# Optimization experiments

Hardware: AMD Instinct MI355X
Metric: run time of the kernel (lower is better)

Reference implementation:

```python
import jax, jax.numpy as jnp
from jax import lax
import numpy as np

B, FRAMES, H, W = 8, 128, 64, 64
N_MFCC = 60
VID_FEAT = 196
D = VID_FEAT + N_MFCC   # COMBINE_SIZE = 256
ED = 2 * D              # mamba d_inner = 512
NST = 16                # d_state
DTR = 16                # dt_rank = ceil(D/16)
NL = 4                  # layers per direction
NC = 2                  # num_classes


def setup_inputs() -> dict:
    key = jax.random.key(0)
    ks = iter(jax.random.split(key, 64))
    def rn(shape, s=0.02):
        return jax.random.normal(next(ks), shape, jnp.float32) * s
    inp = {
        'video_input': jax.random.normal(next(ks), (B, FRAMES, 3, H, W), jnp.float32),
        'audio_input': jax.random.normal(next(ks), (B, FRAMES * N_MFCC), jnp.float32),
        'cnn_conv1_w': rn((32, 3, 3, 3), 0.1), 'cnn_conv1_b': jnp.zeros((32,), jnp.float32),
        'cnn_conv2_w': rn((64, 32, 3, 3), 0.05), 'cnn_conv2_b': jnp.zeros((64,), jnp.float32),
        'cnn_fc_w': rn((VID_FEAT, 64), 0.1), 'cnn_fc_b': jnp.zeros((VID_FEAT,), jnp.float32),
    }
    for pref in ('fwd', 'bwd'):
        inp[pref + '_norm_w'] = jnp.ones((NL, D), jnp.float32)
        inp[pref + '_in_proj_w'] = rn((NL, 2 * ED, D))
        inp[pref + '_conv_w'] = rn((NL, ED, 4), 0.1)
        inp[pref + '_conv_b'] = jnp.zeros((NL, ED), jnp.float32)
        inp[pref + '_x_proj_w'] = rn((NL, DTR + 2 * NST, ED))
        inp[pref + '_dt_w'] = rn((NL, ED, DTR), 0.1)
        inp[pref + '_dt_b'] = jnp.zeros((NL, ED), jnp.float32)
        inp[pref + '_A_log'] = jnp.tile(jnp.log(jnp.arange(1, NST + 1, dtype=jnp.float32)), (NL, ED, 1))
        inp[pref + '_D'] = jnp.ones((NL, ED), jnp.float32)
        inp[pref + '_out_proj_w'] = rn((NL, D, ED))
    inp['fc_w'] = rn((D, 2 * D)); inp['fc_b'] = jnp.zeros((D,), jnp.float32)
    inp['fc2_w'] = rn((NC, D)); inp['fc2_b'] = jnp.zeros((NC,), jnp.float32)
    return inp


def _rmsnorm(x, w, eps=1e-5):
    return x * lax.rsqrt(jnp.mean(x * x, -1, keepdims=True) + eps) * w


def _conv2d(x, w, b):
    y = lax.conv_general_dilated(x, w, (1, 1), 'SAME', dimension_numbers=('NCHW', 'OIHW', 'NCHW'))
    return y + b[None, :, None, None]


def _maxpool2(x):
    return lax.reduce_window(x, -jnp.inf, lax.max, (1, 1, 2, 2), (1, 1, 2, 2), 'VALID')


def _video_cnn(x, w1, b1, w2, b2, fw, fb):
    x = _maxpool2(jax.nn.relu(_conv2d(x, w1, b1)))
    x = _maxpool2(jax.nn.relu(_conv2d(x, w2, b2)))
    x = jnp.mean(x, (2, 3))            # global avg pool -> [B*F, 64]
    return x @ fw.T + fb               # [B*F, VID_FEAT]


def _mamba_layer(x, norm_w, in_w, conv_w, conv_b, xp_w, dt_w, dt_b, A_log, Dp, out_w):
    Bsz, L, _ = x.shape
    xn = _rmsnorm(x, norm_w)
    xz = jnp.einsum('bld,ed->ble', xn, in_w)        # [B,L,2*ED]
    xc, z = jnp.split(xz, 2, axis=-1)
    # causal depthwise conv1d, kernel 4
    xpad = jnp.pad(xc, ((0, 0), (3, 0), (0, 0)))
    xc = sum(xpad[:, k:k + L, :] * conv_w[:, k] for k in range(4)) + conv_b
    xc = jax.nn.silu(xc)
    dbc = jnp.einsum('ble,re->blr', xc, xp_w)       # [B,L,DTR+2*NST]
    dt, Bm, Cm = dbc[..., :DTR], dbc[..., DTR:DTR + NST], dbc[..., DTR + NST:]
    delta = jax.nn.softplus(jnp.einsum('blr,er->ble', dt, dt_w) + dt_b)  # [B,L,ED]
    A = -jnp.exp(A_log)                             # [ED,NST]
    dA = jnp.exp(delta[..., None] * A)              # [B,L,ED,NST]
    dBx = delta[..., None] * Bm[:, :, None, :] * xc[..., None]
    def step(h, inp):
        dA_t, dBx_t, c_t = inp
        h = dA_t * h + dBx_t
        return h, jnp.einsum('ben,bn->be', h, c_t)
    h0 = jnp.zeros((Bsz, ED, NST), x.dtype)
    _, ys = lax.scan(step, h0, (dA.transpose(1, 0, 2, 3), dBx.transpose(1, 0, 2, 3), Cm.transpose(1, 0, 2)))
    y = ys.transpose(1, 0, 2) + Dp * xc
    y = y * jax.nn.silu(z)
    return x + jnp.einsum('ble,de->bld', y, out_w)


def _mamba(x, norm_w, in_w, conv_w, conv_b, xp_w, dt_w, dt_b, A_log, Dp, out_w):
    for l in range(NL):
        x = _mamba_layer(x, norm_w[l], in_w[l], conv_w[l], conv_b[l], xp_w[l],
                         dt_w[l], dt_b[l], A_log[l], Dp[l], out_w[l])
    return x


def reference(video_input, audio_input, cnn_conv1_w, cnn_conv1_b, cnn_conv2_w, cnn_conv2_b,
              cnn_fc_w, cnn_fc_b,
              fwd_norm_w, fwd_in_proj_w, fwd_conv_w, fwd_conv_b, fwd_x_proj_w, fwd_dt_w,
              fwd_dt_b, fwd_A_log, fwd_D, fwd_out_proj_w,
              bwd_norm_w, bwd_in_proj_w, bwd_conv_w, bwd_conv_b, bwd_x_proj_w, bwd_dt_w,
              bwd_dt_b, bwd_A_log, bwd_D, bwd_out_proj_w,
              fc_w, fc_b, fc2_w, fc2_b):
    bsz, frames = video_input.shape[0], video_input.shape[1]
    xv = video_input.reshape(bsz * frames, 3, H, W)
    xv = _video_cnn(xv, cnn_conv1_w, cnn_conv1_b, cnn_conv2_w, cnn_conv2_b, cnn_fc_w, cnn_fc_b)
    xv = xv.reshape(bsz, frames, VID_FEAT)
    xa = audio_input.reshape(bsz, -1, N_MFCC)       # [B, frames, N_MFCC]
    xc = jnp.concatenate([xv, xa], axis=-1)         # [B, frames, D]
    xf = _mamba(xc, fwd_norm_w, fwd_in_proj_w, fwd_conv_w, fwd_conv_b, fwd_x_proj_w,
                fwd_dt_w, fwd_dt_b, fwd_A_log, fwd_D, fwd_out_proj_w)
    xb = _mamba(xc[:, ::-1], bwd_norm_w, bwd_in_proj_w, bwd_conv_w, bwd_conv_b, bwd_x_proj_w,
                bwd_dt_w, bwd_dt_b, bwd_A_log, bwd_D, bwd_out_proj_w)[:, ::-1]
    x_last = jnp.concatenate([xf, xb], axis=-1)[:, -1, :]   # [B, 2*D]; dropout = identity (eval)
    x = x_last @ fc_w.T + fc_b
    return x @ fc2_w.T + fc2_b
```

## Files before the change

kernel.cpp:

```cpp
#include <hip/hip_runtime.h>
#include <hip/hip_bf16.h>
#include <cstdint>
#include <cstddef>

#define BATCH 8
#define FRAMES 128
#define TOK (BATCH*FRAMES)
#define NM 60
#define VF 196
#define DD 256
#define EDIM 512
#define NSTATE 16
#define DTRANK 16
#define NLAYER 4

typedef __attribute__((ext_vector_type(8))) short short8v;
typedef __attribute__((ext_vector_type(4))) float f32x4;

__device__ __forceinline__ unsigned short f2bf(float f) {
  unsigned x = __float_as_uint(f);
  unsigned r = (x + 0x7FFFu + ((x >> 16) & 1u)) >> 16;
  return (unsigned short)r;
}

__global__ void pack_w2(const float* __restrict__ w2, unsigned short* __restrict__ Wb,
                        const float* __restrict__ w1, unsigned short* __restrict__ Wb1) {
  int id = blockIdx.x * 256 + threadIdx.x;
  if (id < 9 * 4 * 64) {
    int lane = id & 63;
    int mt = (id >> 6) & 3;
    int sh = id >> 8;
    int dy = sh / 3, dx = sh % 3;
    int oc = mt * 16 + (lane & 15);
    int ic0 = (lane >> 4) * 8;
    unsigned u[4];
#pragma unroll
    for (int p = 0; p < 4; ++p) {
      unsigned short lo = f2bf(w2[((oc * 32 + ic0 + 2 * p) * 3 + dy) * 3 + dx]);
      unsigned short hi = f2bf(w2[((oc * 32 + ic0 + 2 * p + 1) * 3 + dy) * 3 + dx]);
      u[p] = (unsigned)lo | ((unsigned)hi << 16);
    }
    uint4 v = {u[0], u[1], u[2], u[3]};
    *(uint4*)(Wb + (size_t)id * 8) = v;
  } else if (id < 9 * 4 * 64 + 128) {
    int id2 = id - 9 * 4 * 64;
    int mt = id2 >> 6, lane = id2 & 63;
    int oc = mt * 16 + (lane & 15);
    int ko = lane >> 4;
    unsigned u[4];
#pragma unroll
    for (int p = 0; p < 4; ++p) {
      int k0 = ko * 8 + 2 * p, k1 = k0 + 1;
      unsigned short lo = (k0 < 27) ? f2bf(w1[oc * 27 + k0]) : 0;
      unsigned short hi = (k1 < 27) ? f2bf(w1[oc * 27 + k1]) : 0;
      u[p] = (unsigned)lo | ((unsigned)hi << 16);
    }
    uint4 v = {u[0], u[1], u[2], u[3]};
    *(uint4*)(Wb1 + (size_t)id2 * 8) = v;
  }
}

__global__ void pack_mamba(const float* __restrict__ ipF, const float* __restrict__ ipR,
                           const float* __restrict__ opF, const float* __restrict__ opR,
                           const float* __restrict__ xpF, const float* __restrict__ xpR,
                           unsigned short* __restrict__ Wip, unsigned short* __restrict__ Wop,
                           unsigned short* __restrict__ Wxp) {
  int id = blockIdx.x * 256 + threadIdx.x;
  if (id < 262144) {
    int dl = id >> 15, r = id & 32767;
    int ntile = r >> 9, kt = (r >> 6) & 7, lane = r & 63;
    int dir = dl >> 2, layer = dl & 3;
    const float* src = (dir ? ipR : ipF) + (size_t)layer * 1024 * 256
                       + (size_t)(ntile * 16 + (lane & 15)) * 256 + kt * 32 + (lane >> 4) * 8;
    unsigned u[4];
#pragma unroll
    for (int p = 0; p < 4; ++p)
      u[p] = (unsigned)f2bf(src[2 * p]) | ((unsigned)f2bf(src[2 * p + 1]) << 16);
    uint4 v = {u[0], u[1], u[2], u[3]};
    *(uint4*)(Wip + (size_t)id * 8) = v;
  } else if (id < 262144 + 131072) {
    int id2 = id - 262144;
    int dl = id2 >> 14, rr = id2 & 16383;
    int ntile = rr >> 10, kt = (rr >> 6) & 15, lane = rr & 63;
    int dir = dl >> 2, layer = dl & 3;
    const float* src = (dir ? opR : opF) + (size_t)layer * 256 * 512
                       + (size_t)(ntile * 16 + (lane & 15)) * 512 + kt * 32 + (lane >> 4) * 8;
    unsigned u[4];
#pragma unroll
    for (int p = 0; p < 4; ++p)
      u[p] = (unsigned)f2bf(src[2 * p]) | ((unsigned)f2bf(src[2 * p + 1]) << 16);
    uint4 v = {u[0], u[1], u[2], u[3]};
    *(uint4*)(Wop + (size_t)id2 * 8) = v;
  } else if (id < 262144 + 131072 + 24576) {
    int id3 = id - 262144 - 131072;
    int dl = id3 / 3072, rr = id3 % 3072;
    int ntile = rr >> 10, kt = (rr >> 6) & 15, lane = rr & 63;
    int dir = dl >> 2, layer = dl & 3;
    const float* src = (dir ? xpR : xpF) + (size_t)layer * 48 * 512
                       + (size_t)(ntile * 16 + (lane & 15)) * 512 + kt * 32 + (lane >> 4) * 8;
    unsigned u[4];
#pragma unroll
    for (int p = 0; p < 4; ++p)
      u[p] = (unsigned)f2bf(src[2 * p]) | ((unsigned)f2bf(src[2 * p + 1]) << 16);
    uint4 v = {u[0], u[1], u[2], u[3]};
    *(uint4*)(Wxp + (size_t)id3 * 8) = v;
  }
}

#define C1RS 68
#define C1ICS (66*68)
__global__ __launch_bounds__(256) void conv1_mfma(
    const float* __restrict__ video, const unsigned short* __restrict__ Wb1,
    const float* __restrict__ b1, unsigned short* __restrict__ X1)
{
  __shared__ unsigned short ldsu[3 * C1ICS + 96];
  const int img = blockIdx.x, t = threadIdx.x;
  const float* vin = video + (size_t)img * 12288;
  const int lane = t & 63, wv = t >> 6;
  const int col = lane & 15, ko = lane >> 4;

  for (int i = t; i < (3 * C1ICS + 96) / 2; i += 256) ((unsigned*)ldsu)[i] = 0;
  __syncthreads();
#pragma unroll
  for (int i = 0; i < 12; ++i) {
    int c = i * 256 + t;
    int ic = c >> 10, rem = c & 1023, gy = rem >> 4, c4 = rem & 15;
    float4 v = *(const float4*)(vin + ic * 4096 + gy * 64 + c4 * 4);
    unsigned lo = (unsigned)f2bf(v.x) | ((unsigned)f2bf(v.y) << 16);
    unsigned hi = (unsigned)f2bf(v.z) | ((unsigned)f2bf(v.w) << 16);
    int di = ic * C1ICS + (gy + 1) * C1RS + 4 + c4 * 4;
    *(uint2*)(ldsu + di) = (uint2){lo, hi};
  }

  short8v A0 = *(const short8v*)(Wb1 + (size_t)(0 * 64 + lane) * 8);
  short8v A1 = *(const short8v*)(Wb1 + (size_t)(1 * 64 + lane) * 8);
  float bia[2][4];
#pragma unroll
  for (int mt = 0; mt < 2; ++mt)
#pragma unroll
    for (int r = 0; r < 4; ++r) bia[mt][r] = b1[mt * 16 + ko * 4 + r];

  int offs[8];
#pragma unroll
  for (int j = 0; j < 8; ++j) {
    int k = ko * 8 + j;
    int o = 0;
    if (k < 27) {
      int ic = k / 9, tap = k - ic * 9;
      int dy = tap / 3, dx = tap - dy * 3;
      o = ic * C1ICS + dy * C1RS + dx + 3;
    }
    offs[j] = o;
  }
  __syncthreads();

  f32x4 z4 = {0.f, 0.f, 0.f, 0.f};
#pragma unroll 1
  for (int rp = 0; rp < 8; ++rp) {
    const int y0 = wv * 16 + rp * 2;
#pragma unroll
    for (int xg = 0; xg < 4; ++xg) {
      const int bse = y0 * C1RS + xg * 16 + col;
      short8v vb0, vb1;
#pragma unroll
      for (int j = 0; j < 8; ++j) {
        vb0[j] = (short)ldsu[bse + offs[j]];
        vb1[j] = (short)ldsu[bse + C1RS + offs[j]];
      }
      f32x4 c00 = __builtin_amdgcn_mfma_f32_16x16x32_bf16(A0, vb0, z4, 0, 0, 0);
      f32x4 c10 = __builtin_amdgcn_mfma_f32_16x16x32_bf16(A1, vb0, z4, 0, 0, 0);
      f32x4 c01 = __builtin_amdgcn_mfma_f32_16x16x32_bf16(A0, vb1, z4, 0, 0, 0);
      f32x4 c11 = __builtin_amdgcn_mfma_f32_16x16x32_bf16(A1, vb1, z4, 0, 0, 0);
      const int py = wv * 8 + rp;
      const int pxp = xg * 8 + (col >> 1);
#pragma unroll
      for (int mt = 0; mt < 2; ++mt) {
        f32x4 ca = mt ? c10 : c00;
        f32x4 cb = mt ? c11 : c01;
        unsigned pk[2];
#pragma unroll
        for (int r = 0; r < 4; ++r) {
          float va = fmaxf(ca[r] + bia[mt][r], 0.f);
          float vb = fmaxf(cb[r] + bia[mt][r], 0.f);
          float v = fmaxf(va, vb);
          v = fmaxf(v, __shfl_xor(v, 1, 64));
          unsigned short u = f2bf(v);
          if ((r & 1) == 0) pk[r >> 1] = (unsigned)u;
          else              pk[r >> 1] |= ((unsigned)u << 16);
        }
        if ((col & 1) == 0) {
          uint2 o = {pk[0], pk[1]};
          *(uint2*)(X1 + ((size_t)(img * 1024 + py * 32 + pxp) * 32 + mt * 16 + ko * 4)) = o;
        }
      }
    }
  }
}

#define X_LDS_BYTES (4 * 1156 * 16)
#define OCT_STRIDE  (1156 * 16)
__global__ __launch_bounds__(256) void conv2_k(
    const unsigned short* __restrict__ X1, const unsigned short* __restrict__ Wb,
    const float* __restrict__ b2, float* __restrict__ feat)
{
  extern __shared__ char sm[];
  float* part = (float*)(sm + X_LDS_BYTES);
  const int img = blockIdx.x, t = threadIdx.x;
  const int lane = t & 63, wv = t >> 6;
  const int kg = lane >> 4, l15 = lane & 15;

  for (int j = t; j < 1156; j += 256) {
    int r = j / 34, cc = j - r * 34;
    if (r == 0 || r == 33 || cc == 0 || cc == 33) {
      uint4 z = {0, 0, 0, 0};
#pragma unroll
      for (int oct = 0; oct < 4; ++oct)
        *(uint4*)(sm + oct * OCT_STRIDE + j * 16) = z;
    }
  }
  const uint4* src = (const uint4*)(X1 + (size_t)img * 32768);
#pragma unroll 4
  for (int i = 0; i < 16; ++i) {
    int c = i * 256 + t;
    uint4 v = src[c];
    int oct = c & 3, P = c >> 2;
    int y = P >> 5, x = P & 31;
    *(uint4*)(sm + oct * OCT_STRIDE + ((y + 1) * 34 + (x + 1)) * 16) = v;
  }
  __syncthreads();

  float bia[4][4];
#pragma unroll
  for (int mt = 0; mt < 4; ++mt)
#pragma unroll
    for (int r = 0; r < 4; ++r) bia[mt][r] = b2[mt * 16 + kg * 4 + r];

  float msum[4][4];
#pragma unroll
  for (int mt = 0; mt < 4; ++mt)
#pragma unroll
    for (int r = 0; r < 4; ++r) msum[mt][r] = 0.f;

#pragma unroll 1
  for (int pass = 0; pass < 2; ++pass) {
    f32x4 acc[4][8];
#pragma unroll
    for (int mt = 0; mt < 4; ++mt)
#pragma unroll
      for (int q = 0; q < 8; ++q) acc[mt][q] = (f32x4){0.f, 0.f, 0.f, 0.f};
    int Pq[8];
#pragma unroll
    for (int q = 0; q < 8; ++q) {
      int p = (wv * 16 + pass * 8 + q) * 16 + l15;
      int y = p >> 5, x = p & 31;
      Pq[q] = y * 34 + x;
    }
#pragma unroll
    for (int sh = 0; sh < 9; ++sh) {
      const int dy = sh / 3, dx = sh % 3;
      const int shoff = (dy * 34 + dx) * 16;
      short8v Af[4];
#pragma unroll
      for (int mt = 0; mt < 4; ++mt)
        Af[mt] = *(const short8v*)(Wb + ((size_t)(sh * 4 + mt) * 64 + lane) * 8);
#pragma unroll
      for (int q = 0; q < 8; ++q) {
        short8v Bf = *(const short8v*)(sm + kg * OCT_STRIDE + Pq[q] * 16 + shoff);
#pragma unroll
        for (int mt = 0; mt < 4; ++mt)
          acc[mt][q] = __builtin_amdgcn_mfma_f32_16x16x32_bf16(Af[mt], Bf, acc[mt][q], 0, 0, 0);
      }
    }
#pragma unroll
    for (int mt = 0; mt < 4; ++mt) {
#pragma unroll
      for (int pr = 0; pr < 4; ++pr) {
        int qa = (pr & 1) + (pr >> 1) * 4;
        int qb = qa + 2;
#pragma unroll
        for (int r = 0; r < 4; ++r) {
          float va = fmaxf(acc[mt][qa][r] + bia[mt][r], 0.f);
          float vb = fmaxf(acc[mt][qb][r] + bia[mt][r], 0.f);
          float v = fmaxf(va, vb);
          v = fmaxf(v, __shfl_xor(v, 1, 64));
          msum[mt][r] += v;
        }
      }
    }
  }
#pragma unroll
  for (int mt = 0; mt < 4; ++mt)
#pragma unroll
    for (int r = 0; r < 4; ++r) {
      float v = msum[mt][r];
      v += __shfl_xor(v, 1, 64);
      v += __shfl_xor(v, 2, 64);
      v += __shfl_xor(v, 4, 64);
      v += __shfl_xor(v, 8, 64);
      if (l15 == 0) part[wv * 64 + mt * 16 + kg * 4 + r] = v * 0.5f;
    }
  __syncthreads();
  if (t < 64)
    feat[(size_t)img * 64 + t] =
        (part[t] + part[64 + t] + part[128 + t] + part[192 + t]) * (1.f / 256.f);
}

__global__ __launch_bounds__(256) void fcgemm_k(
    const float* __restrict__ A, const float* __restrict__ B,
    const float* __restrict__ bias, const float* __restrict__ audio,
    float* __restrict__ xf, float* __restrict__ xr)
{
  __shared__ float sA[16][68];
  __shared__ float sB[16][68];
  const int t = threadIdx.x;
  const int m0 = blockIdx.x * 64;
  const int n0 = blockIdx.y * 64;
  const int tx = t & 15, ty = t >> 4;
  const int lk = t & 15, lr = t >> 4;
  float acc[4][4] = {};
  for (int k0 = 0; k0 < 64; k0 += 16) {
#pragma unroll
    for (int rr = 0; rr < 4; ++rr) {
      int m = m0 + lr + rr * 16;
      sA[lk][lr + rr * 16] = A[(size_t)m * 64 + k0 + lk];
      int n = n0 + lr + rr * 16;
      sB[lk][lr + rr * 16] = (n < VF) ? B[(size_t)n * 64 + k0 + lk] : 0.f;
    }
    __syncthreads();
#pragma unroll
    for (int kk = 0; kk < 16; ++kk) {
      float a0 = sA[kk][ty*4+0], a1 = sA[kk][ty*4+1], a2 = sA[kk][ty*4+2], a3 = sA[kk][ty*4+3];
      float b0 = sB[kk][tx*4+0], b1 = sB[kk][tx*4+1], b2 = sB[kk][tx*4+2], b3 = sB[kk][tx*4+3];
      acc[0][0]=fmaf(a0,b0,acc[0][0]); acc[0][1]=fmaf(a0,b1,acc[0][1]); acc[0][2]=fmaf(a0,b2,acc[0][2]); acc[0][3]=fmaf(a0,b3,acc[0][3]);
      acc[1][0]=fmaf(a1,b0,acc[1][0]); acc[1][1]=fmaf(a1,b1,acc[1][1]); acc[1][2]=fmaf(a1,b2,acc[1][2]); acc[1][3]=fmaf(a1,b3,acc[1][3]);
      acc[2][0]=fmaf(a2,b0,acc[2][0]); acc[2][1]=fmaf(a2,b1,acc[2][1]); acc[2][2]=fmaf(a2,b2,acc[2][2]); acc[2][3]=fmaf(a2,b3,acc[2][3]);
      acc[3][0]=fmaf(a3,b0,acc[3][0]); acc[3][1]=fmaf(a3,b1,acc[3][1]); acc[3][2]=fmaf(a3,b2,acc[3][2]); acc[3][3]=fmaf(a3,b3,acc[3][3]);
    }
    __syncthreads();
  }
#pragma unroll
  for (int i = 0; i < 4; ++i) {
    int m = m0 + ty * 4 + i;
    int b = m >> 7, l = m & 127;
    int mr = (b << 7) + (127 - l);
#pragma unroll
    for (int j = 0; j < 4; ++j) {
      int n = n0 + tx * 4 + j;
      float v;
      if (n < VF)       v = acc[i][j] + bias[n];
      else              v = audio[(size_t)b * (FRAMES * NM) + l * NM + (n - VF)];
      xf[(size_t)m * DD + n] = v;
      xr[(size_t)mr * DD + n] = v;
    }
  }
}

__global__ __launch_bounds__(256) void inproj_mfma3(
    const float* __restrict__ xF, const float* __restrict__ xR,
    const float* __restrict__ nwF, const float* __restrict__ nwR,
    const unsigned short* __restrict__ Wip, int layer,
    float* __restrict__ xzF, float* __restrict__ xzR)
{
  const int dir = blockIdx.z;
  const float* x = dir ? xR : xF;
  const float* nw = dir ? nwR : nwF;
  float* xz = dir ? xzR : xzF;
  __shared__ unsigned short sa[32 * 16 * 8];
  const int t = threadIdx.x;
  const int tok0 = blockIdx.x * 16;
  {
    const int tk = t >> 4, l16 = t & 15;
    const float* row = x + (size_t)(tok0 + tk) * DD + l16 * 16;
    float v[16];
    float ss = 0.f;
#pragma unroll
    for (int i = 0; i < 4; ++i) {
      float4 f = ((const float4*)row)[i];
      v[4*i] = f.x; v[4*i+1] = f.y; v[4*i+2] = f.z; v[4*i+3] = f.w;
      ss += f.x*f.x + f.y*f.y + f.z*f.z + f.w*f.w;
    }
    ss += __shfl_xor(ss, 1, 16);
    ss += __shfl_xor(ss, 2, 16);
    ss += __shfl_xor(ss, 4, 16);
    ss += __shfl_xor(ss, 8, 16);
    float scale = rsqrtf(ss * (1.f / DD) + 1e-5f);
    const float* nwp = nw + l16 * 16;
#pragma unroll
    for (int hh = 0; hh < 2; ++hh) {
      unsigned ub[4];
#pragma unroll
      for (int p = 0; p < 4; ++p) {
        unsigned short lo = f2bf(v[hh*8 + 2*p]     * scale * nwp[hh*8 + 2*p]);
        unsigned short hi = f2bf(v[hh*8 + 2*p + 1] * scale * nwp[hh*8 + 2*p + 1]);
        ub[p] = (unsigned)lo | ((unsigned)hi << 16);
      }
      int k0 = l16 * 16 + hh * 8;
      int kt = k0 >> 5, oct = (k0 >> 3) & 3;
      uint4 w4 = {ub[0], ub[1], ub[2], ub[3]};
      *(uint4*)(sa + ((size_t)(kt * 4 + oct) * 16 + tk) * 8) = w4;
    }
  }
  __syncthreads();
  const int lane = t & 63, w = t >> 6;
  short8v af[8];
#pragma unroll
  for (int kt = 0; kt < 8; ++kt)
    af[kt] = *(const short8v*)(sa + ((size_t)(kt * 4 + (lane >> 4)) * 16 + (lane & 15)) * 8);
#pragma unroll
  for (int ns = 0; ns < 4; ++ns) {
    const int ntile = blockIdx.y * 16 + w * 4 + ns;
    const unsigned short* wb = Wip + (((size_t)(dir * 4 + layer) * 512 + ntile * 8) * 64 + lane) * 8;
    f32x4 acc = (f32x4){0.f, 0.f, 0.f, 0.f};
#pragma unroll
    for (int kt = 0; kt < 8; ++kt) {
      short8v bf = *(const short8v*)(wb + (size_t)kt * 64 * 8);
      acc = __builtin_amdgcn_mfma_f32_16x16x32_bf16(af[kt], bf, acc, 0, 0, 0);
    }
#pragma unroll
    for (int r = 0; r < 4; ++r)
      xz[(size_t)(tok0 + (lane >> 4) * 4 + r) * 1024 + ntile * 16 + (lane & 15)] = acc[r];
  }
}

__global__ __launch_bounds__(256) void convsilu2_k(
    const float* __restrict__ xzF, const float* __restrict__ xzR,
    const float* __restrict__ cwF, const float* __restrict__ cwR,
    const float* __restrict__ cbF, const float* __restrict__ cbR,
    float* __restrict__ xcF, float* __restrict__ xcR,
    unsigned short* __restrict__ xcbF, unsigned short* __restrict__ xcbR)
{
  const int dir = blockIdx.z;
  const float* xz = dir ? xzR : xzF;
  const float* cw = dir ? cwR : cwF;
  const float* cb = dir ? cbR : cbF;
  float* xc = dir ? xcR : xcF;
  unsigned short* xcb = dir ? xcbR : xcbF;

  int i = blockIdx.x * 256 + threadIdx.x;
  int tok = i >> 6;
  int e0 = (i & 63) << 3;
  int l = tok & 127;
  const float* col = xz + (size_t)tok * 1024 + e0;

  float v3[8] = {}, v2[8] = {}, v1[8] = {}, v0[8];
  if (l >= 3) { *(float4*)v3 = *(const float4*)(col - 3072); *(float4*)(v3+4) = *(const float4*)(col - 3068); }
  if (l >= 2) { *(float4*)v2 = *(const float4*)(col - 2048); *(float4*)(v2+4) = *(const float4*)(col - 2044); }
  if (l >= 1) { *(float4*)v1 = *(const float4*)(col - 1024); *(float4*)(v1+4) = *(const float4*)(col - 1020); }
  *(float4*)v0 = *(const float4*)col; *(float4*)(v0+4) = *(const float4*)(col + 4);

  float cbv[8];
  *(float4*)cbv = *(const float4*)(cb + e0); *(float4*)(cbv+4) = *(const float4*)(cb + e0 + 4);

  float res[8];
#pragma unroll
  for (int j = 0; j < 8; ++j) {
    float4 cv = ((const float4*)cw)[e0 + j];
    float a = cbv[j];
    a = fmaf(cv.x, v3[j], a);
    a = fmaf(cv.y, v2[j], a);
    a = fmaf(cv.z, v1[j], a);
    a = fmaf(cv.w, v0[j], a);
    res[j] = a / (1.f + __expf(-a));
  }
  float4 r0 = {res[0], res[1], res[2], res[3]};
  float4 r1 = {res[4], res[5], res[6], res[7]};
  float* xcp = xc + (size_t)tok * EDIM + e0;
  *(float4*)xcp = r0; *(float4*)(xcp + 4) = r1;

  unsigned ub[4];
#pragma unroll
  for (int p = 0; p < 4; ++p)
    ub[p] = (unsigned)f2bf(res[2*p]) | ((unsigned)f2bf(res[2*p+1]) << 16);
  int kt = e0 >> 5, oct = (e0 >> 3) & 3;
  uint4 w4 = {ub[0], ub[1], ub[2], ub[3]};
  *(uint4*)(xcb + ((size_t)(kt * 4 + oct) * 1024 + tok) * 8) = w4;
}

__global__ __launch_bounds__(64) void xproj_mfma(
    const unsigned short* __restrict__ xcbF, const unsigned short* __restrict__ xcbR,
    const unsigned short* __restrict__ Wxp, int layer,
    float* __restrict__ dbF, float* __restrict__ dbR)
{
  const int dir = blockIdx.z;
  const unsigned short* xcb = dir ? xcbR : xcbF;
  float* db = dir ? dbR : dbF;
  const int lane = threadIdx.x & 63;
  const int tok0 = blockIdx.x * 16;
  const unsigned short* wbase = Wxp + ((size_t)(dir * 4 + layer) * 3 * 16 * 64) * 8;
  f32x4 acc[3];
#pragma unroll
  for (int nt = 0; nt < 3; ++nt) acc[nt] = (f32x4){0.f, 0.f, 0.f, 0.f};
#pragma unroll
  for (int kt = 0; kt < 16; ++kt) {
    short8v af = *(const short8v*)(xcb + ((size_t)(kt * 4 + (lane >> 4)) * 1024 + tok0 + (lane & 15)) * 8);
#pragma unroll
    for (int nt = 0; nt < 3; ++nt) {
      short8v bf = *(const short8v*)(wbase + ((size_t)(nt * 16 + kt) * 64 + lane) * 8);
      acc[nt] = __builtin_amdgcn_mfma_f32_16x16x32_bf16(af, bf, acc[nt], 0, 0, 0);
    }
  }
#pragma unroll
  for (int nt = 0; nt < 3; ++nt)
#pragma unroll
    for (int r = 0; r < 4; ++r)
      db[(size_t)(tok0 + (lane >> 4) * 4 + r) * 48 + nt * 16 + (lane & 15)] = acc[nt][r];
}

__global__ __launch_bounds__(256) void scan4_k(
    const float* __restrict__ xzF, const float* __restrict__ xzR,
    const float* __restrict__ xcF, const float* __restrict__ xcR,
    const float* __restrict__ dbF, const float* __restrict__ dbR,
    const float* __restrict__ dwF, const float* __restrict__ dwR,
    const float* __restrict__ dtbF, const float* __restrict__ dtbR,
    const float* __restrict__ AlF, const float* __restrict__ AlR,
    const float* __restrict__ DpF, const float* __restrict__ DpR,
    unsigned short* __restrict__ yoF, unsigned short* __restrict__ yoR)
{
  const int dir = blockIdx.z;
  const float* xz = dir ? xzR : xzF;
  const float* xc = dir ? xcR : xcF;
  const float* db = dir ? dbR : dbF;
  const float* dw = dir ? dwR : dwF;
  const float* dtbv = dir ? dtbR : dtbF;
  const float* Al = dir ? AlR : AlF;
  const float* Dp = dir ? DpR : DpF;
  unsigned short* yo = dir ? yoR : yoF;

  __shared__ float sdb[FRAMES * 48];
  __shared__ float sxc[FRAMES * 16];
  __shared__ float sgz[FRAMES * 16];
  __shared__ float sdl[FRAMES * 16];
  const int b = blockIdx.x >> 5;
  const int e0 = (blockIdx.x & 31) << 4;
  const int t = threadIdx.x, g = t >> 4, n = t & 15;
  const int e = e0 + g;

  const float* dbp = db + (size_t)b * FRAMES * 48;
  for (int i = t; i < FRAMES * 48 / 4; i += 256)
    ((float4*)sdb)[i] = ((const float4*)dbp)[i];
  for (int i = t; i < FRAMES * 16; i += 256) {
    int l = i >> 4, c = i & 15;
    int ee = e0 + c;
    sxc[i] = xc[(size_t)(b * FRAMES + l) * EDIM + ee];
    float zz = xz[(size_t)(b * FRAMES + l) * 1024 + 512 + ee];
    sgz[i] = zz / (1.f + __expf(-zz));
    const float* d = db + (size_t)(b * FRAMES + l) * 48;
    const float* w = dw + (size_t)ee * 16;
    float a = dtbv[ee];
#pragma unroll
    for (int q = 0; q < 4; ++q) {
      float4 dv = *(const float4*)(d + 4 * q);
      float4 wv = *(const float4*)(w + 4 * q);
      a = fmaf(dv.x, wv.x, a); a = fmaf(dv.y, wv.y, a);
      a = fmaf(dv.z, wv.z, a); a = fmaf(dv.w, wv.w, a);
    }
    sdl[i] = (a > 20.f) ? a : __logf(1.f + __expf(a));
  }
  float An = -expf(Al[e * NSTATE + n]);
  float Dv = Dp[e];
  float h = 0.f;
  unsigned short* yp = yo + ((size_t)((e >> 5) * 4 + ((e >> 3) & 3)) * 1024 + b * FRAMES) * 8 + (e & 7);
  __syncthreads();

#pragma unroll 1
  for (int l = 0; l < FRAMES; ++l) {
    float dlt = sdl[l * 16 + g];
    float xcv = sxc[l * 16 + g];
    float Bn = sdb[l * 48 + 16 + n];
    float Cn = sdb[l * 48 + 32 + n];
    float dA = __expf(dlt * An);
    h = fmaf(dA, h, dlt * xcv * Bn);
    float part = h * Cn;
    part += __shfl_xor(part, 1, 16);
    part += __shfl_xor(part, 2, 16);
    part += __shfl_xor(part, 4, 16);
    part += __shfl_xor(part, 8, 16);
    if (n == 0) {
      float a2 = fmaf(Dv, xcv, part);
      yp[(size_t)l * 8] = f2bf(a2 * sgz[l * 16 + g]);
    }
  }
}

__global__ __launch_bounds__(256) void outproj_mfma(
    const unsigned short* __restrict__ yoF, const unsigned short* __restrict__ yoR,
    const unsigned short* __restrict__ Wop, int layer,
    float* __restrict__ xF, float* __restrict__ xR)
{
  const int dir = blockIdx.z;
  const unsigned short* yo = dir ? yoR : yoF;
  float* xx = dir ? xR : xF;
  const int t = threadIdx.x, lane = t & 63, w = t >> 6;
  const int m0 = blockIdx.x * 32, n0 = blockIdx.y * 64;
  const int ntile = blockIdx.y * 4 + w;
  const unsigned short* wb = Wop + (((size_t)(dir * 4 + layer) * 256 + ntile * 16) * 64 + lane) * 8;
  f32x4 acc[2];
  acc[0] = (f32x4){0.f, 0.f, 0.f, 0.f};
  acc[1] = (f32x4){0.f, 0.f, 0.f, 0.f};
#pragma unroll
  for (int kt = 0; kt < 16; ++kt) {
    short8v bf = *(const short8v*)(wb + (size_t)kt * 64 * 8);
#pragma unroll
    for (int mt = 0; mt < 2; ++mt) {
      short8v af = *(const short8v*)(yo + ((size_t)(kt * 4 + (lane >> 4)) * 1024 + m0 + mt * 16 + (lane & 15)) * 8);
      acc[mt] = __builtin_amdgcn_mfma_f32_16x16x32_bf16(af, bf, acc[mt], 0, 0, 0);
    }
  }
#pragma unroll
  for (int mt = 0; mt < 2; ++mt)
#pragma unroll
    for (int r = 0; r < 4; ++r) {
      size_t ci = (size_t)(m0 + mt * 16 + (lane >> 4) * 4 + r) * DD + n0 + w * 16 + (lane & 15);
      xx[ci] += acc[mt][r];
    }
}

__global__ __launch_bounds__(256) void head_k(
    const float* __restrict__ xf, const float* __restrict__ xr,
    const float* __restrict__ fcw, const float* __restrict__ fcb,
    const float* __restrict__ fc2w, const float* __restrict__ fc2b,
    float* __restrict__ out)
{
  int b = blockIdx.x;
  __shared__ float xl[2 * DD];
  __shared__ float h[DD];
  __shared__ float hp[4];
  int t = threadIdx.x;
  xl[t]      = xf[(size_t)(b * FRAMES + FRAMES - 1) * DD + t];
  xl[DD + t] = xr[(size_t)(b * FRAMES + 0) * DD + t];
  __syncthreads();
  float acc = fcb[t];
  for (int k = 0; k < 2 * DD; ++k) acc = fmaf(xl[k], fcw[(size_t)t * 2 * DD + k], acc);
  h[t] = acc;
  __syncthreads();
  {
    int c = t >> 7, k = t & 127;
    float p = h[k] * fc2w[c * DD + k] + h[k + 128] * fc2w[c * DD + k + 128];
#pragma unroll
    for (int off = 32; off; off >>= 1) p += __shfl_xor(p, off, 64);
    if ((t & 63) == 0) hp[t >> 6] = p;
  }
  __syncthreads();
  if (t < 2) out[b * 2 + t] = hp[2 * t] + hp[2 * t + 1] + fc2b[t];
}

extern "C" void kernel_launch(void* const* d_in, const int* in_sizes, int n_in,
                              void* d_out, int out_size, void* d_ws, size_t ws_size,
                              hipStream_t stream) {
  const float* video = (const float*)d_in[0];
  const float* audio = (const float*)d_in[1];
  const float* c1w = (const float*)d_in[2];
  const float* c1b = (const float*)d_in[3];
  const float* c2w = (const float*)d_in[4];
  const float* c2b = (const float*)d_in[5];
  const float* fcw = (const float*)d_in[6];
  const float* fcb = (const float*)d_in[7];
  const float* Wf[10]; const float* Wb_[10];
  for (int i = 0; i < 10; ++i) { Wf[i] = (const float*)d_in[8+i]; Wb_[i] = (const float*)d_in[18+i]; }
  const float* fc_w  = (const float*)d_in[28];
  const float* fc_b  = (const float*)d_in[29];
  const float* fc2_w = (const float*)d_in[30];
  const float* fc2_b = (const float*)d_in[31];
  float* out = (float*)d_out;

  float* ws   = (float*)d_ws;
  float* feat = ws;
  float* xf   = feat + 65536;
  float* xr   = xf   + 262144;
  float* xzF  = xr   + 262144;
  float* xzR  = xzF  + 1048576;
  float* xcF  = xzR  + 1048576;
  float* xcR  = xcF  + 524288;
  float* dbF  = xcR  + 524288;
  float* dbR  = dbF  + 49152;
  unsigned short* yoF = (unsigned short*)(dbR + 49152);
  unsigned short* yoR = yoF + 524288;
  unsigned short* X1  = yoR + 524288;
  unsigned short* Wbp = X1 + 33554432;
  unsigned short* Wip = Wbp + 18432;
  unsigned short* Wop = Wip + 2097152;
  unsigned short* Wxp = Wop + 1048576;
  unsigned short* xcbF = Wxp + 196608;
  unsigned short* xcbR = xcbF + 524288;
  unsigned short* Wb1  = xcbR + 524288;

  pack_w2<<<dim3(10), 256, 0, stream>>>(c2w, Wbp, c1w, Wb1);
  pack_mamba<<<dim3(1632), 256, 0, stream>>>(Wf[1], Wb_[1], Wf[9], Wb_[9], Wf[4], Wb_[4],
                                             Wip, Wop, Wxp);
  conv1_mfma<<<dim3(TOK), 256, 0, stream>>>(video, Wb1, c1b, X1);
  conv2_k<<<dim3(TOK), 256, (size_t)(X_LDS_BYTES + 1024), stream>>>(X1, Wbp, c2b, feat);

  fcgemm_k<<<dim3(16, 4), 256, 0, stream>>>(feat, fcw, fcb, audio, xf, xr);

  for (int l = 0; l < NLAYER; ++l) {
    const float* nwF  = Wf[0] + l*DD;              const float* nwR  = Wb_[0] + l*DD;
    const float* cwF_ = Wf[2] + l*EDIM*4;          const float* cwR_ = Wb_[2] + l*EDIM*4;
    const float* cbF_ = Wf[3] + l*EDIM;            const float* cbR_ = Wb_[3] + l*EDIM;
    const float* dwF  = Wf[5] + l*EDIM*DTRANK;     const float* dwR  = Wb_[5] + l*EDIM*DTRANK;
    const float* dtbF = Wf[6] + l*EDIM;            const float* dtbR = Wb_[6] + l*EDIM;
    const float* AlF  = Wf[7] + l*EDIM*NSTATE;     const float* AlR  = Wb_[7] + l*EDIM*NSTATE;
    const float* DpF  = Wf[8] + l*EDIM;            const float* DpR  = Wb_[8] + l*EDIM;

    inproj_mfma3<<<dim3(64, 4, 2), 256, 0, stream>>>(xf, xr, nwF, nwR, Wip, l, xzF, xzR);
    convsilu2_k<<<dim3(256, 1, 2), 256, 0, stream>>>(xzF, xzR, cwF_, cwR_, cbF_, cbR_,
                                                     xcF, xcR, xcbF, xcbR);
    xproj_mfma<<<dim3(64, 1, 2), 64, 0, stream>>>(xcbF, xcbR, Wxp, l, dbF, dbR);
    scan4_k<<<dim3(256, 1, 2), 256, 0, stream>>>(xzF, xzR, xcF, xcR, dbF, dbR, dwF, dwR,
                                                 dtbF, dtbR, AlF, AlR, DpF, DpR, yoF, yoR);
    outproj_mfma<<<dim3(32, 4, 2), 256, 0, stream>>>(yoF, yoR, Wop, l, xf, xr);
  }

  head_k<<<dim3(BATCH), 256, 0, stream>>>(xf, xr, fc_w, fc_b, fc2_w, fc2_b, out);
}
```

Measured before the change: 383.6 us.

## Fuse conv+SiLU into x_proj GEMM via LDS; split conv2 accumulators to cut registers

The depthwise conv+SiLU kernel and the x_proj MFMA kernel are merged into one kernel per layer. It computes the bf16 activations for 16 tokens into swizzled shared memory and runs the x_proj MFMAs from there, which removes the global bf16 staging buffer and one launch per layer. Only 3 of the 4 waves do the MFMA phase, and the grid shrinks to 128 blocks, so the conv+SiLU part runs with less parallelism. Separately, the conv2 kernel splits each pass into two halves with 4 accumulator tiles instead of 8, lowering register pressure at the cost of more loop iterations and reloading the weight fragments.

```diff
diff --git a/kernel.cpp b/kernel.cpp
--- a/kernel.cpp
+++ b/kernel.cpp
@@ -243,47 +243,49 @@
 
 #pragma unroll 1
   for (int pass = 0; pass < 2; ++pass) {
-    f32x4 acc[4][8];
-#pragma unroll
-    for (int mt = 0; mt < 4; ++mt)
-#pragma unroll
-      for (int q = 0; q < 8; ++q) acc[mt][q] = (f32x4){0.f, 0.f, 0.f, 0.f};
-    int Pq[8];
-#pragma unroll
-    for (int q = 0; q < 8; ++q) {
-      int p = (wv * 16 + pass * 8 + q) * 16 + l15;
-      int y = p >> 5, x = p & 31;
-      Pq[q] = y * 34 + x;
-    }
-#pragma unroll
-    for (int sh = 0; sh < 9; ++sh) {
-      const int dy = sh / 3, dx = sh % 3;
-      const int shoff = (dy * 34 + dx) * 16;
-      short8v Af[4];
+#pragma unroll 1
+    for (int hf = 0; hf < 2; ++hf) {
+      f32x4 acc[4][4];
 #pragma unroll
       for (int mt = 0; mt < 4; ++mt)
-        Af[mt] = *(const short8v*)(Wb + ((size_t)(sh * 4 + mt) * 64 + lane) * 8);
-#pragma unroll
-      for (int q = 0; q < 8; ++q) {
-        short8v Bf = *(const short8v*)(sm + kg * OCT_STRIDE + Pq[q] * 16 + shoff);
+#pragma unroll
+        for (int q = 0; q < 4; ++q) acc[mt][q] = (f32x4){0.f, 0.f, 0.f, 0.f};
+      int Pq[4];
+#pragma unroll
+      for (int q = 0; q < 4; ++q) {
+        int p = (wv * 16 + pass * 8 + hf * 4 + q) * 16 + l15;
+        int y = p >> 5, x = p & 31;
+        Pq[q] = y * 34 + x;
+      }
+#pragma unroll
+      for (int sh = 0; sh < 9; ++sh) {
+        const int dy = sh / 3, dx = sh % 3;
+        const int shoff = (dy * 34 + dx) * 16;
+        short8v Af[4];
 #pragma unroll
         for (int mt = 0; mt < 4; ++mt)
-          acc[mt][q] = __builtin_amdgcn_mfma_f32_16x16x32_bf16(Af[mt], Bf, acc[mt][q], 0, 0, 0);
+          Af[mt] = *(const short8v*)(Wb + ((size_t)(sh * 4 + mt) * 64 + lane) * 8);
+#pragma unroll
+        for (int q = 0; q < 4; ++q) {
+          short8v Bf = *(const short8v*)(sm + kg * OCT_STRIDE + Pq[q] * 16 + shoff);
+#pragma unroll
+          for (int mt = 0; mt < 4; ++mt)
+            acc[mt][q] = __builtin_amdgcn_mfma_f32_16x16x32_bf16(Af[mt], Bf, acc[mt][q], 0, 0, 0);
+        }
       }
-    }
-#pragma unroll
-    for (int mt = 0; mt < 4; ++mt) {
-#pragma unroll
-      for (int pr = 0; pr < 4; ++pr) {
-        int qa = (pr & 1) + (pr >> 1) * 4;
-        int qb = qa + 2;
-#pragma unroll
-        for (int r = 0; r < 4; ++r) {
-          float va = fmaxf(acc[mt][qa][r] + bia[mt][r], 0.f);
-          float vb = fmaxf(acc[mt][qb][r] + bia[mt][r], 0.f);
-          float v = fmaxf(va, vb);
-          v = fmaxf(v, __shfl_xor(v, 1, 64));
-          msum[mt][r] += v;
+#pragma unroll
+      for (int mt = 0; mt < 4; ++mt) {
+#pragma unroll
+        for (int pr = 0; pr < 2; ++pr) {
+          int qa = pr, qb = pr + 2;
+#pragma unroll
+          for (int r = 0; r < 4; ++r) {
+            float va = fmaxf(acc[mt][qa][r] + bia[mt][r], 0.f);
+            float vb = fmaxf(acc[mt][qb][r] + bia[mt][r], 0.f);
+            float v = fmaxf(va, vb);
+            v = fmaxf(v, __shfl_xor(v, 1, 64));
+            msum[mt][r] += v;
+          }
         }
       }
     }
@@ -422,88 +424,85 @@
   }
 }
 
-__global__ __launch_bounds__(256) void convsilu2_k(
+__global__ __launch_bounds__(256) void xprojf_k(
     const float* __restrict__ xzF, const float* __restrict__ xzR,
     const float* __restrict__ cwF, const float* __restrict__ cwR,
     const float* __restrict__ cbF, const float* __restrict__ cbR,
+    const unsigned short* __restrict__ Wxp, int layer,
     float* __restrict__ xcF, float* __restrict__ xcR,
-    unsigned short* __restrict__ xcbF, unsigned short* __restrict__ xcbR)
+    float* __restrict__ dbF, float* __restrict__ dbR)
 {
   const int dir = blockIdx.z;
   const float* xz = dir ? xzR : xzF;
   const float* cw = dir ? cwR : cwF;
   const float* cb = dir ? cbR : cbF;
   float* xc = dir ? xcR : xcF;
-  unsigned short* xcb = dir ? xcbR : xcbF;
-
-  int i = blockIdx.x * 256 + threadIdx.x;
-  int tok = i >> 6;
-  int e0 = (i & 63) << 3;
-  int l = tok & 127;
-  const float* col = xz + (size_t)tok * 1024 + e0;
-
-  float v3[8] = {}, v2[8] = {}, v1[8] = {}, v0[8];
-  if (l >= 3) { *(float4*)v3 = *(const float4*)(col - 3072); *(float4*)(v3+4) = *(const float4*)(col - 3068); }
-  if (l >= 2) { *(float4*)v2 = *(const float4*)(col - 2048); *(float4*)(v2+4) = *(const float4*)(col - 2044); }
-  if (l >= 1) { *(float4*)v1 = *(const float4*)(col - 1024); *(float4*)(v1+4) = *(const float4*)(col - 1020); }
-  *(float4*)v0 = *(const float4*)col; *(float4*)(v0+4) = *(const float4*)(col + 4);
-
-  float cbv[8];
-  *(float4*)cbv = *(const float4*)(cb + e0); *(float4*)(cbv+4) = *(const float4*)(cb + e0 + 4);
-
-  float res[8];
-#pragma unroll
-  for (int j = 0; j < 8; ++j) {
-    float4 cv = ((const float4*)cw)[e0 + j];
-    float a = cbv[j];
-    a = fmaf(cv.x, v3[j], a);
-    a = fmaf(cv.y, v2[j], a);
-    a = fmaf(cv.z, v1[j], a);
-    a = fmaf(cv.w, v0[j], a);
-    res[j] = a / (1.f + __expf(-a));
-  }
-  float4 r0 = {res[0], res[1], res[2], res[3]};
-  float4 r1 = {res[4], res[5], res[6], res[7]};
-  float* xcp = xc + (size_t)tok * EDIM + e0;
-  *(float4*)xcp = r0; *(float4*)(xcp + 4) = r1;
-
-  unsigned ub[4];
-#pragma unroll
-  for (int p = 0; p < 4; ++p)
-    ub[p] = (unsigned)f2bf(res[2*p]) | ((unsigned)f2bf(res[2*p+1]) << 16);
-  int kt = e0 >> 5, oct = (e0 >> 3) & 3;
-  uint4 w4 = {ub[0], ub[1], ub[2], ub[3]};
-  *(uint4*)(xcb + ((size_t)(kt * 4 + oct) * 1024 + tok) * 8) = w4;
-}
-
-__global__ __launch_bounds__(64) void xproj_mfma(
-    const unsigned short* __restrict__ xcbF, const unsigned short* __restrict__ xcbR,
-    const unsigned short* __restrict__ Wxp, int layer,
-    float* __restrict__ dbF, float* __restrict__ dbR)
-{
-  const int dir = blockIdx.z;
-  const unsigned short* xcb = dir ? xcbR : xcbF;
   float* db = dir ? dbR : dbF;
-  const int lane = threadIdx.x & 63;
+  __shared__ unsigned short sa[64 * 16 * 8];
+  const int t = threadIdx.x;
   const int tok0 = blockIdx.x * 16;
-  const unsigned short* wbase = Wxp + ((size_t)(dir * 4 + layer) * 3 * 16 * 64) * 8;
-  f32x4 acc[3];
-#pragma unroll
-  for (int nt = 0; nt < 3; ++nt) acc[nt] = (f32x4){0.f, 0.f, 0.f, 0.f};
-#pragma unroll
-  for (int kt = 0; kt < 16; ++kt) {
-    short8v af = *(const short8v*)(xcb + ((size_t)(kt * 4 + (lane >> 4)) * 1024 + tok0 + (lane & 15)) * 8);
-#pragma unroll
-    for (int nt = 0; nt < 3; ++nt) {
+
+#pragma unroll
+  for (int ii = 0; ii < 4; ++ii) {
+    int idx = ii * 256 + t;
+    int tk = idx >> 6, tok = tok0 + tk;
+    int e0 = (idx & 63) << 3;
+    int l = tok & 127;
+    const float* col = xz + (size_t)tok * 1024 + e0;
+
+    float v3[8] = {}, v2[8] = {}, v1[8] = {}, v0[8];
+    if (l >= 3) { *(float4*)v3 = *(const float4*)(col - 3072); *(float4*)(v3+4) = *(const float4*)(col - 3068); }
+    if (l >= 2) { *(float4*)v2 = *(const float4*)(col - 2048); *(float4*)(v2+4) = *(const float4*)(col - 2044); }
+    if (l >= 1) { *(float4*)v1 = *(const float4*)(col - 1024); *(float4*)(v1+4) = *(const float4*)(col - 1020); }
+    *(float4*)v0 = *(const float4*)col; *(float4*)(v0+4) = *(const float4*)(col + 4);
+
+    float cbv[8];
+    *(float4*)cbv = *(const float4*)(cb + e0); *(float4*)(cbv+4) = *(const float4*)(cb + e0 + 4);
+
+    float res[8];
+#pragma unroll
+    for (int j = 0; j < 8; ++j) {
+      float4 cv = ((const float4*)cw)[e0 + j];
+      float a = cbv[j];
+      a = fmaf(cv.x, v3[j], a);
+      a = fmaf(cv.y, v2[j], a);
+      a = fmaf(cv.z, v1[j], a);
+      a = fmaf(cv.w, v0[j], a);
+      res[j] = a / (1.f + __expf(-a));
+    }
+    float4 r0 = {res[0], res[1], res[2], res[3]};
+    float4 r1 = {res[4], res[5], res[6], res[7]};
+    float* xcp = xc + (size_t)tok * EDIM + e0;
+    *(float4*)xcp = r0; *(float4*)(xcp + 4) = r1;
+
+    unsigned ub[4];
+#pragma unroll
+    for (int p = 0; p < 4; ++p)
+      ub[p] = (unsigned)f2bf(res[2*p]) | ((unsigned)f2bf(res[2*p+1]) << 16);
+    int c = (e0 >> 3) * 16 + tk;
+    c ^= (c >> 4) & 15;
+    uint4 w4 = {ub[0], ub[1], ub[2], ub[3]};
+    *(uint4*)(sa + (size_t)c * 8) = w4;
+  }
+  __syncthreads();
+
+  const int w = t >> 6, lane = t & 63;
+  if (w < 3) {
+    const int nt = w;
+    const unsigned short* wbase = Wxp + ((size_t)(dir * 4 + layer) * 3 * 16 * 64) * 8;
+    f32x4 acc = (f32x4){0.f, 0.f, 0.f, 0.f};
+#pragma unroll
+    for (int kt = 0; kt < 16; ++kt) {
+      int c = (kt * 4 + (lane >> 4)) * 16 + (lane & 15);
+      c ^= (c >> 4) & 15;
+      short8v af = *(const short8v*)(sa + (size_t)c * 8);
       short8v bf = *(const short8v*)(wbase + ((size_t)(nt * 16 + kt) * 64 + lane) * 8);
-      acc[nt] = __builtin_amdgcn_mfma_f32_16x16x32_bf16(af, bf, acc[nt], 0, 0, 0);
-    }
-  }
-#pragma unroll
-  for (int nt = 0; nt < 3; ++nt)
+      acc = __builtin_amdgcn_mfma_f32_16x16x32_bf16(af, bf, acc, 0, 0, 0);
+    }
 #pragma unroll
     for (int r = 0; r < 4; ++r)
-      db[(size_t)(tok0 + (lane >> 4) * 4 + r) * 48 + nt * 16 + (lane & 15)] = acc[nt][r];
+      db[(size_t)(tok0 + (lane >> 4) * 4 + r) * 48 + nt * 16 + (lane & 15)] = acc[r];
+  }
 }
 
 __global__ __launch_bounds__(256) void scan4_k(
@@ -680,9 +679,7 @@
   unsigned short* Wip = Wbp + 18432;
   unsigned short* Wop = Wip + 2097152;
   unsigned short* Wxp = Wop + 1048576;
-  unsigned short* xcbF = Wxp + 196608;
-  unsigned short* xcbR = xcbF + 524288;
-  unsigned short* Wb1  = xcbR + 524288;
+  unsigned short* Wb1 = Wxp + 196608;
 
   pack_w2<<<dim3(10), 256, 0, stream>>>(c2w, Wbp, c1w, Wb1);
   pack_mamba<<<dim3(1632), 256, 0, stream>>>(Wf[1], Wb_[1], Wf[9], Wb_[9], Wf[4], Wb_[4],
@@ -702,9 +699,8 @@
     const float* DpF  = Wf[8] + l*EDIM;            const float* DpR  = Wb_[8] + l*EDIM;
 
     inproj_mfma3<<<dim3(64, 4, 2), 256, 0, stream>>>(xf, xr, nwF, nwR, Wip, l, xzF, xzR);
-    convsilu2_k<<<dim3(256, 1, 2), 256, 0, stream>>>(xzF, xzR, cwF_, cwR_, cbF_, cbR_,
-                                                     xcF, xcR, xcbF, xcbR);
-    xproj_mfma<<<dim3(64, 1, 2), 64, 0, stream>>>(xcbF, xcbR, Wxp, l, dbF, dbR);
+    xprojf_k<<<dim3(64, 1, 2), 256, 0, stream>>>(xzF, xzR, cwF_, cwR_, cbF_, cbR_,
+                                                 Wxp, l, xcF, xcR, dbF, dbR);
     scan4_k<<<dim3(256, 1, 2), 256, 0, stream>>>(xzF, xzR, xcF, xcR, dbF, dbR, dwF, dwR,
                                                  dtbF, dtbR, AlF, AlR, DpF, DpR, yoF, yoR);
     outproj_mfma<<<dim3(32, 4, 2), 256, 0, stream>>>(yoF, yoR, Wop, l, xf, xr);
```

Result: faster. 364.6 us (-5.0%).
